# Kernel tuning notes

Measured on AMD Instinct MI355X. Metric: run time of the kernel, lower is better.

Reference implementation:

```python
import jax, jax.numpy as jnp
import numpy as np

TAU = 1.0
REDUCTION = 'mean'


def setup_inputs() -> dict:
    key = jax.random.key(0)
    k1, k2 = jax.random.split(key)
    n, d, n_classes = 8192, 128, 100
    projection = jax.random.normal(k1, (n, d), dtype=jnp.float32)
    y = jax.random.randint(k2, (n,), 0, n_classes, dtype=jnp.int64)
    return {"projection": projection, "y": y}


def reference(projection, y):
    n = projection.shape[0]
    sim = projection @ projection.T  # [n, n]
    eq = y[:, None] == y[None, :]
    same_mask = eq & ~jnp.eye(n, dtype=bool)  # same class, excluding self
    diff_mask = ~eq

    big = jnp.asarray(jnp.inf, dtype=sim.dtype)
    # masked per-row min over same-class sims (0 if row has none)
    min_same = jnp.min(jnp.where(same_mask, sim, big), axis=1)
    min_same = jnp.where(jnp.any(same_mask, axis=1), min_same, 0.0)
    # masked per-row max over diff-class sims (0 if row has none)
    max_diff = jnp.max(jnp.where(diff_mask, sim, -big), axis=1)
    max_diff = jnp.where(jnp.any(diff_mask, axis=1), max_diff, 0.0)

    loss_i = jnp.maximum(0.0, min_same + max_diff + TAU)  # [n]
    if REDUCTION == 'mean':
        return jnp.mean(loss_i)
    return jnp.sum(loss_i)
```

## Files before the change

### kernel.cpp

```cpp
#include <hip/hip_runtime.h>
#include <hip/hip_bf16.h>
#include <float.h>

#define N 8192
#define D 128
#define NCLS 100
#define BM 256
#define BN 64
#define GY 16
#define COLS_PER_BLOCK (N / GY)
#define TILES (COLS_PER_BLOCK / BN)
#define NPART GY
#define LOSS_BLOCKS (N / 256)

typedef unsigned short u16;
typedef unsigned int u32;
typedef __attribute__((ext_vector_type(8))) short bf16x8;
typedef __attribute__((ext_vector_type(4))) float f32x4;

typedef const __attribute__((address_space(1))) u32 glb_u32;
typedef __attribute__((address_space(3))) u32 lds_u32;

__device__ __forceinline__ u32 pack_bf16x2(float a, float b) {
  u32 ua = __float_as_uint(a); ua += 0x7FFFu + ((ua >> 16) & 1u);
  u32 ub = __float_as_uint(b); ub += 0x7FFFu + ((ub >> 16) & 1u);
  return (ua >> 16) | (ub & 0xFFFF0000u);
}

__global__ __launch_bounds__(256) void sort_kernel(const int* __restrict__ y,
                                                   int* __restrict__ perm,
                                                   int* __restrict__ yp,
                                                   int* __restrict__ rs,
                                                   int* __restrict__ re) {
  const int c    = blockIdx.x;
  const int ww   = threadIdx.x >> 6;
  const int lane = threadIdx.x & 63;
  const int base0 = ww * (N / 4);

  int lt = 0, eq = 0;
#pragma unroll 2
  for (int i = 0; i < N / 4; i += 256) {
    int v0 = y[base0 + i + lane];
    int v1 = y[base0 + i + 64 + lane];
    int v2 = y[base0 + i + 128 + lane];
    int v3 = y[base0 + i + 192 + lane];
    lt += (v0 < c) + (v1 < c) + (v2 < c) + (v3 < c);
    eq += (v0 == c) + (v1 == c) + (v2 == c) + (v3 == c);
  }
#pragma unroll
  for (int off = 32; off >= 1; off >>= 1) {
    lt += __shfl_down(lt, off, 64);
    eq += __shfl_down(eq, off, 64);
  }
  __shared__ int ltW[4], eqW[4];
  if (lane == 0) { ltW[ww] = lt; eqW[ww] = eq; }
  __syncthreads();
  const int start = ltW[0] + ltW[1] + ltW[2] + ltW[3];
  const int cnt   = eqW[0] + eqW[1] + eqW[2] + eqW[3];
  const int end   = start + cnt;
  int run = start;
  for (int w2 = 0; w2 < ww; ++w2) run += eqW[w2];

  const unsigned long long below = (lane == 0) ? 0ull : ((1ull << lane) - 1ull);
#pragma unroll 2
  for (int i = 0; i < N / 4; i += 128) {
    int v0 = y[base0 + i + lane];
    int v1 = y[base0 + i + 64 + lane];
    unsigned long long m0 = __ballot(v0 == c);
    unsigned long long m1 = __ballot(v1 == c);
    if (v0 == c) {
      int pos = run + __popcll(m0 & below);
      perm[pos] = base0 + i + lane; yp[pos] = c; rs[pos] = start; re[pos] = end;
    }
    run += __popcll(m0);
    if (v1 == c) {
      int pos = run + __popcll(m1 & below);
      perm[pos] = base0 + i + 64 + lane; yp[pos] = c; rs[pos] = start; re[pos] = end;
    }
    run += __popcll(m1);
  }
}

__global__ __launch_bounds__(256) void gather_kernel(const float* __restrict__ P,
                                                     const int* __restrict__ perm,
                                                     u16* __restrict__ Pp) {
  const int rloc = threadIdx.x >> 4;
  const int t16  = threadIdx.x & 15;
  const int k    = blockIdx.x * 16 + rloc;
  const int src  = perm[k];
  const float4* s = reinterpret_cast<const float4*>(P + (size_t)src * D) + t16 * 2;
  float4 v0 = s[0], v1 = s[1];
  uint4 o;
  o.x = pack_bf16x2(v0.x, v0.y);
  o.y = pack_bf16x2(v0.z, v0.w);
  o.z = pack_bf16x2(v1.x, v1.y);
  o.w = pack_bf16x2(v1.z, v1.w);
  reinterpret_cast<uint4*>(Pp + (size_t)k * D)[t16] = o;
}

__global__ __launch_bounds__(256) void margin_main(const u16* __restrict__ Pp,
                                                   const int* __restrict__ yp,
                                                   const int* __restrict__ rs,
                                                   const int* __restrict__ re,
                                                   float* __restrict__ pmin,
                                                   float* __restrict__ pmax) {
  __shared__ __align__(16) char ldsB[3][BN * 256];
  __shared__ int ldsY[COLS_PER_BLOCK];

  const int tid  = threadIdx.x;
  const int w    = tid >> 6;
  const int lane = tid & 63;
  const int c15  = lane & 15;
  const int g    = lane >> 4;

  const int R0 = blockIdx.x * BM;
  const int C0 = blockIdx.y * COLS_PER_BLOCK;
  const char* pbb = (const char*)Pp;

  {
    const int* gy = yp + C0 + w * 128 + lane;
    lds_u32* dst = (lds_u32*)(ldsY + w * 128);
    __builtin_amdgcn_global_load_lds((glb_u32*)gy,        dst,      4, 0, 0);
    __builtin_amdgcn_global_load_lds((glb_u32*)(gy + 64), dst + 64, 4, 0, 0);
  }

  auto STAGE = [&](int buf, int t) {
    const char* gb = pbb + (size_t)(C0 + t * BN) * 256;
    char* base = &ldsB[buf][0];
#pragma unroll
    for (int j = 0; j < 4; ++j) {
      const int L = ((w * 4 + j) * 64 + lane) * 16;
      const int c = L >> 8, o = L & 255;
      const int src = c * 256 + (o ^ ((c & 15) << 4));
      __builtin_amdgcn_global_load_lds((glb_u32*)(gb + src),
                                       (lds_u32*)(base + (w * 4 + j) * 1024), 16, 0, 0);
    }
  };

  STAGE(0, 0);
  STAGE(1, 1);

  const int R0w = R0 + w * 64;
  const int stripLo = __builtin_amdgcn_readfirstlane(rs[R0w]);
  const int stripHi = __builtin_amdgcn_readfirstlane(re[R0w + 63]);

  bf16x8 afrag[4][4];
#pragma unroll
  for (int rg = 0; rg < 4; ++rg) {
    const char* ap = pbb + (size_t)(R0w + rg * 16 + c15) * 256 + g * 16;
#pragma unroll
    for (int kk = 0; kk < 4; ++kk)
      afrag[rg][kk] = *reinterpret_cast<const bf16x8*>(ap + kk * 64);
  }
  int yrow[4][4];
#pragma unroll
  for (int rg = 0; rg < 4; ++rg)
#pragma unroll
    for (int r = 0; r < 4; ++r)
      yrow[rg][r] = yp[R0w + rg * 16 + g * 4 + r];

  float rmin[4][4], rmax[4][4];
#pragma unroll
  for (int rg = 0; rg < 4; ++rg)
#pragma unroll
    for (int r = 0; r < 4; ++r) { rmin[rg][r] = FLT_MAX; rmax[rg][r] = -FLT_MAX; }

#pragma unroll 1
  for (int t = 0; t < TILES; ++t) {
    if (t + 1 < TILES) asm volatile("s_waitcnt vmcnt(4)" ::: "memory");
    else               asm volatile("s_waitcnt vmcnt(0)" ::: "memory");
    __builtin_amdgcn_s_barrier();
    if (t + 2 < TILES) STAGE((t + 2) % 3, t + 2);

    const char* Bb = &ldsB[t % 3][0];
#pragma unroll
    for (int s = 0; s < 4; ++s) {
      const int c = s * 16 + c15;
      bf16x8 bf[4];
#pragma unroll
      for (int kk = 0; kk < 4; ++kk) {
        const int off = c * 256 + (((g * 16) | (kk * 64)) ^ (c15 << 4));
        bf[kk] = *reinterpret_cast<const bf16x8*>(Bb + off);
      }
      f32x4 acc[4];
#pragma unroll
      for (int rg = 0; rg < 4; ++rg) acc[rg] = (f32x4){0.f, 0.f, 0.f, 0.f};
      __builtin_amdgcn_s_setprio(1);
#pragma unroll
      for (int kk = 0; kk < 4; ++kk)
#pragma unroll
        for (int rg = 0; rg < 4; ++rg)
          acc[rg] = __builtin_amdgcn_mfma_f32_16x16x32_bf16(afrag[rg][kk], bf[kk],
                                                            acc[rg], 0, 0, 0);
      __builtin_amdgcn_s_setprio(0);

      const int colT = C0 + t * BN + s * 16;
      if (colT + 16 <= stripLo || colT >= stripHi) {
#pragma unroll
        for (int rg = 0; rg < 4; ++rg)
#pragma unroll
          for (int r = 0; r < 4; ++r)
            rmax[rg][r] = fmaxf(rmax[rg][r], acc[rg][r]);
      } else {
        const int ycol = ldsY[t * BN + s * 16 + c15];
        const int colg = colT + c15;
#pragma unroll
        for (int rg = 0; rg < 4; ++rg)
#pragma unroll
          for (int r = 0; r < 4; ++r) {
            const float v = acc[rg][r];
            const bool same = (ycol == yrow[rg][r]);
            const bool okmin = same && (colg != R0w + rg * 16 + g * 4 + r);
            rmin[rg][r] = fminf(rmin[rg][r], okmin ? v : FLT_MAX);
            rmax[rg][r] = fmaxf(rmax[rg][r], same ? -FLT_MAX : v);
          }
      }
    }
  }

#pragma unroll
  for (int off = 1; off < 16; off <<= 1)
#pragma unroll
    for (int rg = 0; rg < 4; ++rg)
#pragma unroll
      for (int r = 0; r < 4; ++r) {
        rmin[rg][r] = fminf(rmin[rg][r], __shfl_xor(rmin[rg][r], off, 64));
        rmax[rg][r] = fmaxf(rmax[rg][r], __shfl_xor(rmax[rg][r], off, 64));
      }

  if (c15 == 0) {
#pragma unroll
    for (int rg = 0; rg < 4; ++rg)
#pragma unroll
      for (int r = 0; r < 4; ++r) {
        const int row = R0w + rg * 16 + g * 4 + r;
        pmin[(size_t)blockIdx.y * N + row] = rmin[rg][r];
        pmax[(size_t)blockIdx.y * N + row] = rmax[rg][r];
      }
  }
}

__global__ __launch_bounds__(256) void loss_kernel(const float* __restrict__ pmin,
                                                   const float* __restrict__ pmax,
                                                   float* __restrict__ blockSums) {
  const int row = blockIdx.x * 256 + threadIdx.x;
  float mn = FLT_MAX, mx = -FLT_MAX;
#pragma unroll
  for (int s = 0; s < NPART; ++s) {
    mn = fminf(mn, pmin[(size_t)s * N + row]);
    mx = fmaxf(mx, pmax[(size_t)s * N + row]);
  }
  if (mn == FLT_MAX)  mn = 0.f;
  if (mx == -FLT_MAX) mx = 0.f;
  float loss = fmaxf(0.f, mn + mx + 1.0f);

#pragma unroll
  for (int off = 32; off >= 1; off >>= 1)
    loss += __shfl_down(loss, off, 64);
  __shared__ float wsum[4];
  if ((threadIdx.x & 63) == 0) wsum[threadIdx.x >> 6] = loss;
  __syncthreads();
  if (threadIdx.x == 0)
    blockSums[blockIdx.x] = wsum[0] + wsum[1] + wsum[2] + wsum[3];
}

__global__ __launch_bounds__(64) void finalize_kernel(const float* __restrict__ blockSums,
                                                      float* __restrict__ out) {
  float v = (threadIdx.x < LOSS_BLOCKS) ? blockSums[threadIdx.x] : 0.f;
#pragma unroll
  for (int off = 32; off >= 1; off >>= 1)
    v += __shfl_down(v, off, 64);
  if (threadIdx.x == 0) out[0] = v / (float)N;
}

extern "C" void kernel_launch(void* const* d_in, const int* in_sizes, int n_in,
                              void* d_out, int out_size, void* d_ws, size_t ws_size,
                              hipStream_t stream) {
  const float* P = (const float*)d_in[0];
  const int*   y = (const int*)d_in[1];
  float* out = (float*)d_out;

  u16* Pp   = (u16*)d_ws;
  int* perm = (int*)((char*)d_ws + (size_t)N * D * sizeof(u16));
  int* yp   = perm + N;
  int* rs   = yp + N;
  int* re   = rs + N;
  float* pmin = (float*)(re + N);
  float* pmax = pmin + (size_t)N * NPART;
  float* blockSums = pmax + (size_t)N * NPART;

  sort_kernel<<<dim3(NCLS), 256, 0, stream>>>(y, perm, yp, rs, re);
  gather_kernel<<<dim3(N / 16), 256, 0, stream>>>(P, perm, Pp);
  margin_main<<<dim3(N / BM, GY), 256, 0, stream>>>(Pp, yp, rs, re, pmin, pmax);
  loss_kernel<<<dim3(LOSS_BLOCKS), 256, 0, stream>>>(pmin, pmax, blockSums);
  finalize_kernel<<<1, 64, 0, stream>>>(blockSums, out);
}
```

Before: 46.50 us.

## Split margin block across eight waves with barrier-synchronized MFMA phases

```diff
diff --git a/kernel.cpp b/kernel.cpp
--- a/kernel.cpp
+++ b/kernel.cpp
@@ -98,7 +98,7 @@
   reinterpret_cast<uint4*>(Pp + (size_t)k * D)[t16] = o;
 }
 
-__global__ __launch_bounds__(256) void margin_main(const u16* __restrict__ Pp,
+__global__ __launch_bounds__(512) void margin_main(const u16* __restrict__ Pp,
                                                    const int* __restrict__ yp,
                                                    const int* __restrict__ rs,
                                                    const int* __restrict__ re,
@@ -116,62 +116,56 @@
   const int R0 = blockIdx.x * BM;
   const int C0 = blockIdx.y * COLS_PER_BLOCK;
   const char* pbb = (const char*)Pp;
-
-  {
-    const int* gy = yp + C0 + w * 128 + lane;
-    lds_u32* dst = (lds_u32*)(ldsY + w * 128);
-    __builtin_amdgcn_global_load_lds((glb_u32*)gy,        dst,      4, 0, 0);
-    __builtin_amdgcn_global_load_lds((glb_u32*)(gy + 64), dst + 64, 4, 0, 0);
-  }
+  const int R0w = R0 + w * 32;
+
+  bf16x8 afrag[2][4];
+#pragma unroll
+  for (int rg = 0; rg < 2; ++rg) {
+    const char* ap = pbb + (size_t)(R0w + rg * 16 + c15) * 256 + g * 16;
+#pragma unroll
+    for (int kk = 0; kk < 4; ++kk)
+      afrag[rg][kk] = *reinterpret_cast<const bf16x8*>(ap + kk * 64);
+  }
+  int yrow[2][4];
+#pragma unroll
+  for (int rg = 0; rg < 2; ++rg)
+#pragma unroll
+    for (int r = 0; r < 4; ++r)
+      yrow[rg][r] = yp[R0w + rg * 16 + g * 4 + r];
+  const int stripLo = __builtin_amdgcn_readfirstlane(rs[R0w]);
+  const int stripHi = __builtin_amdgcn_readfirstlane(re[R0w + 31]);
 
   auto STAGE = [&](int buf, int t) {
     const char* gb = pbb + (size_t)(C0 + t * BN) * 256;
     char* base = &ldsB[buf][0];
 #pragma unroll
-    for (int j = 0; j < 4; ++j) {
-      const int L = ((w * 4 + j) * 64 + lane) * 16;
+    for (int j = 0; j < 2; ++j) {
+      const int L = ((w * 2 + j) * 64 + lane) * 16;
       const int c = L >> 8, o = L & 255;
       const int src = c * 256 + (o ^ ((c & 15) << 4));
       __builtin_amdgcn_global_load_lds((glb_u32*)(gb + src),
-                                       (lds_u32*)(base + (w * 4 + j) * 1024), 16, 0, 0);
+                                       (lds_u32*)(base + (w * 2 + j) * 1024), 16, 0, 0);
     }
   };
 
+  __builtin_amdgcn_sched_barrier(0);
+  __builtin_amdgcn_global_load_lds((glb_u32*)(yp + C0 + w * 64 + lane),
+                                   (lds_u32*)(ldsY + w * 64), 4, 0, 0);
   STAGE(0, 0);
   STAGE(1, 1);
-
-  const int R0w = R0 + w * 64;
-  const int stripLo = __builtin_amdgcn_readfirstlane(rs[R0w]);
-  const int stripHi = __builtin_amdgcn_readfirstlane(re[R0w + 63]);
-
-  bf16x8 afrag[4][4];
-#pragma unroll
-  for (int rg = 0; rg < 4; ++rg) {
-    const char* ap = pbb + (size_t)(R0w + rg * 16 + c15) * 256 + g * 16;
-#pragma unroll
-    for (int kk = 0; kk < 4; ++kk)
-      afrag[rg][kk] = *reinterpret_cast<const bf16x8*>(ap + kk * 64);
-  }
-  int yrow[4][4];
-#pragma unroll
-  for (int rg = 0; rg < 4; ++rg)
-#pragma unroll
-    for (int r = 0; r < 4; ++r)
-      yrow[rg][r] = yp[R0w + rg * 16 + g * 4 + r];
-
-  float rmin[4][4], rmax[4][4];
-#pragma unroll
-  for (int rg = 0; rg < 4; ++rg)
+  __builtin_amdgcn_sched_barrier(0);
+
+  float rmin[2][4], rmax[2][4];
+#pragma unroll
+  for (int rg = 0; rg < 2; ++rg)
 #pragma unroll
     for (int r = 0; r < 4; ++r) { rmin[rg][r] = FLT_MAX; rmax[rg][r] = -FLT_MAX; }
 
 #pragma unroll 1
   for (int t = 0; t < TILES; ++t) {
-    if (t + 1 < TILES) asm volatile("s_waitcnt vmcnt(4)" ::: "memory");
+    if (t + 1 < TILES) asm volatile("s_waitcnt vmcnt(2)" ::: "memory");
     else               asm volatile("s_waitcnt vmcnt(0)" ::: "memory");
     __builtin_amdgcn_s_barrier();
-    if (t + 2 < TILES) STAGE((t + 2) % 3, t + 2);
-
     const char* Bb = &ldsB[t % 3][0];
 #pragma unroll
     for (int s = 0; s < 4; ++s) {
@@ -182,33 +176,36 @@
         const int off = c * 256 + (((g * 16) | (kk * 64)) ^ (c15 << 4));
         bf[kk] = *reinterpret_cast<const bf16x8*>(Bb + off);
       }
-      f32x4 acc[4];
-#pragma unroll
-      for (int rg = 0; rg < 4; ++rg) acc[rg] = (f32x4){0.f, 0.f, 0.f, 0.f};
+      if (s == 0 && t + 2 < TILES) STAGE((t + 2) % 3, t + 2);
+
+      __builtin_amdgcn_s_barrier();
+
+      f32x4 acc0 = {0.f, 0.f, 0.f, 0.f}, acc1 = {0.f, 0.f, 0.f, 0.f};
       __builtin_amdgcn_s_setprio(1);
 #pragma unroll
-      for (int kk = 0; kk < 4; ++kk)
-#pragma unroll
-        for (int rg = 0; rg < 4; ++rg)
-          acc[rg] = __builtin_amdgcn_mfma_f32_16x16x32_bf16(afrag[rg][kk], bf[kk],
-                                                            acc[rg], 0, 0, 0);
+      for (int kk = 0; kk < 4; ++kk) {
+        acc0 = __builtin_amdgcn_mfma_f32_16x16x32_bf16(afrag[0][kk], bf[kk], acc0, 0, 0, 0);
+        acc1 = __builtin_amdgcn_mfma_f32_16x16x32_bf16(afrag[1][kk], bf[kk], acc1, 0, 0, 0);
+      }
       __builtin_amdgcn_s_setprio(0);
+
+      __builtin_amdgcn_s_barrier();
 
       const int colT = C0 + t * BN + s * 16;
       if (colT + 16 <= stripLo || colT >= stripHi) {
 #pragma unroll
-        for (int rg = 0; rg < 4; ++rg)
-#pragma unroll
-          for (int r = 0; r < 4; ++r)
-            rmax[rg][r] = fmaxf(rmax[rg][r], acc[rg][r]);
+        for (int r = 0; r < 4; ++r) {
+          rmax[0][r] = fmaxf(rmax[0][r], acc0[r]);
+          rmax[1][r] = fmaxf(rmax[1][r], acc1[r]);
+        }
       } else {
         const int ycol = ldsY[t * BN + s * 16 + c15];
         const int colg = colT + c15;
 #pragma unroll
-        for (int rg = 0; rg < 4; ++rg)
+        for (int rg = 0; rg < 2; ++rg)
 #pragma unroll
           for (int r = 0; r < 4; ++r) {
-            const float v = acc[rg][r];
+            const float v = (rg == 0) ? acc0[r] : acc1[r];
             const bool same = (ycol == yrow[rg][r]);
             const bool okmin = same && (colg != R0w + rg * 16 + g * 4 + r);
             rmin[rg][r] = fminf(rmin[rg][r], okmin ? v : FLT_MAX);
@@ -221,7 +218,7 @@
 #pragma unroll
   for (int off = 1; off < 16; off <<= 1)
 #pragma unroll
-    for (int rg = 0; rg < 4; ++rg)
+    for (int rg = 0; rg < 2; ++rg)
 #pragma unroll
       for (int r = 0; r < 4; ++r) {
         rmin[rg][r] = fminf(rmin[rg][r], __shfl_xor(rmin[rg][r], off, 64));
@@ -230,7 +227,7 @@
 
   if (c15 == 0) {
 #pragma unroll
-    for (int rg = 0; rg < 4; ++rg)
+    for (int rg = 0; rg < 2; ++rg)
 #pragma unroll
       for (int r = 0; r < 4; ++r) {
         const int row = R0w + rg * 16 + g * 4 + r;
@@ -291,7 +288,7 @@
 
   sort_kernel<<<dim3(NCLS), 256, 0, stream>>>(y, perm, yp, rs, re);
   gather_kernel<<<dim3(N / 16), 256, 0, stream>>>(P, perm, Pp);
-  margin_main<<<dim3(N / BM, GY), 256, 0, stream>>>(Pp, yp, rs, re, pmin, pmax);
+  margin_main<<<dim3(N / BM, GY), 512, 0, stream>>>(Pp, yp, rs, re, pmin, pmax);
   loss_kernel<<<dim3(LOSS_BLOCKS), 256, 0, stream>>>(pmin, pmax, blockSums);
   finalize_kernel<<<1, 64, 0, stream>>>(blockSums, out);
 }
```

Measured after the change: 42.79 us. 8.0% less time.
